# Kernel tuning notes

Measured on AMD Instinct MI355X. Metric: run time of the kernel, lower is better.

## Reference

```python
import jax, jax.numpy as jnp
import numpy as np

N_NODES = 50000
N_EDGES = 400000
IN_DIM = 256
HID = 64
N_CLASSES = 121


def setup_inputs() -> dict:
    key = jax.random.key(0)
    ks = jax.random.split(key, 16)
    inp = {
        "features": jax.random.normal(ks[0], (N_NODES, IN_DIM), jnp.float32),
        "src": jax.random.randint(ks[1], (N_EDGES,), 0, N_NODES, jnp.int32),
        "dst": jax.random.randint(ks[2], (N_EDGES,), 0, N_NODES, jnp.int32),
        # layer 0: 4 heads, in_dim -> hid, no residual
        "W0": jax.random.normal(ks[3], (4, HID, IN_DIM), jnp.float32) * 0.05,
        "al0": jax.random.normal(ks[4], (4, HID), jnp.float32) * 0.05,
        "ar0": jax.random.normal(ks[5], (4, HID), jnp.float32) * 0.05,
        # layer 1: 4 heads, 4*hid -> hid, residual via fc
        "W1": jax.random.normal(ks[6], (4, HID, 4 * HID), jnp.float32) * 0.05,
        "al1": jax.random.normal(ks[7], (4, HID), jnp.float32) * 0.05,
        "ar1": jax.random.normal(ks[8], (4, HID), jnp.float32) * 0.05,
        "R1": jax.random.normal(ks[9], (4, HID, 4 * HID), jnp.float32) * 0.05,
        # final: 6 heads, 4*hid -> classes, residual via fc, averaged
        "Wf": jax.random.normal(ks[10], (6, N_CLASSES, 4 * HID), jnp.float32) * 0.05,
        "alf": jax.random.normal(ks[11], (6, N_CLASSES), jnp.float32) * 0.05,
        "arf": jax.random.normal(ks[12], (6, N_CLASSES), jnp.float32) * 0.05,
        "Rf": jax.random.normal(ks[13], (6, N_CLASSES, 4 * HID), jnp.float32) * 0.05,
    }
    return inp


def _gat_layer(x, src, dst, W, al, ar, R, n_nodes):
    """Multi-head GAT layer. x:[N,D], W:[H,K,D], al/ar:[H,K], R:[H,K,D] or None.
    Returns [N,H,K] = activation(residual + edge-softmax-weighted neighbor sum)."""
    ft = jnp.einsum('nd,hkd->nhk', x, W)              # [N,H,K]
    a1 = jnp.einsum('nhk,hk->nh', ft, al)             # [N,H] attn_l(ft)
    a2 = jnp.einsum('nhk,hk->nh', ft, ar)             # [N,H] attn_r(ft)
    # per-edge score: leaky_relu(a1[dst] + a2[src]) (DGL mailbox softmax over in-edges)
    s = jax.nn.leaky_relu(a1[dst] + a2[src], negative_slope=0.01)   # [E,H]
    smax = jax.ops.segment_max(s, dst, num_segments=n_nodes)        # [N,H]
    smax = jnp.where(jnp.isfinite(smax), smax, 0.0)
    ex = jnp.exp(s - smax[dst])                                     # [E,H]
    denom = jax.ops.segment_sum(ex, dst, num_segments=n_nodes)      # [N,H]
    msg = ex[:, :, None] * ft[src]                                  # [E,H,K]
    accum = jax.ops.segment_sum(msg, dst, num_segments=n_nodes)     # [N,H,K]
    accum = accum / jnp.where(denom > 0, denom, 1.0)[:, :, None]
    if R is not None:
        accum = accum + jnp.einsum('nd,hkd->nhk', x, R)
    return jax.nn.elu(accum)


def reference(features, src, dst, W0, al0, ar0, W1, al1, ar1, R1, Wf, alf, arf, Rf):
    n = features.shape[0]
    h0 = _gat_layer(features, src, dst, W0, al0, ar0, None, n)  # [N,4,64]
    h0 = h0.reshape(n, -1)                                      # concat heads -> [N,256]
    h1 = _gat_layer(h0, src, dst, W1, al1, ar1, R1, n)          # [N,4,64]
    h1 = h1.reshape(n, -1)                                      # [N,256]
    hf = _gat_layer(h1, src, dst, Wf, alf, arf, Rf, n)          # [N,6,121]
    return hf.mean(axis=1)                                      # average final heads -> [N,121]
```

## Files before the change

### kernel.cpp

```cpp
#include <hip/hip_runtime.h>
#include <math.h>

#define NN 50000
#define NE 400000
#define NB ((NN + 255) / 256)

typedef __attribute__((ext_vector_type(8))) short bf16x8;
typedef __attribute__((ext_vector_type(4))) float f32x4;
#define AS1 __attribute__((address_space(1)))
#define AS3 __attribute__((address_space(3)))

__device__ __forceinline__ float lrelu(float x){ return x > 0.0f ? x : 0.01f*x; }
__device__ __forceinline__ float eluf(float x){ return x > 0.0f ? x : __expf(x)-1.0f; }
__device__ __forceinline__ float bf2f(unsigned short u){
  union{unsigned i; float f;} v; v.i = ((unsigned)u)<<16; return v.f;
}
__device__ __forceinline__ unsigned short f2bf(float x){
  union{float f; unsigned i;} v; v.f = x;
  unsigned r = v.i + 0x7FFFu + ((v.i>>16)&1u);
  return (unsigned short)(r>>16);
}
__device__ __forceinline__ unsigned pack2(float a, float b){
  return (unsigned)f2bf(a) | ((unsigned)f2bf(b)<<16);
}
__device__ __forceinline__ float lo16(unsigned u){ return bf2f((unsigned short)(u & 0xffffu)); }
__device__ __forceinline__ float hi16(unsigned u){ return bf2f((unsigned short)(u >> 16)); }

__global__ void k_diag(float* out, float val){ out[0] = val; }

__global__ void k_cvt(const float* __restrict__ in, unsigned short* __restrict__ o, int n){
  int i = (blockIdx.x*256 + threadIdx.x)*4;
  if(i + 3 < n){
    float4 v = *(const float4*)(in + i);
    uint2 p; p.x = pack2(v.x, v.y); p.y = pack2(v.z, v.w);
    *(uint2*)(o + i) = p;
  } else {
    for(int k = i; k < n; k++) o[k] = f2bf(in[k]);
  }
}

__global__ void k_cvt3(const float* __restrict__ s0, const float* __restrict__ s1,
    const float* __restrict__ s2, unsigned short* __restrict__ d0,
    unsigned short* __restrict__ d1, unsigned short* __restrict__ d2, int n){
  const float* in = (blockIdx.y == 0) ? s0 : (blockIdx.y == 1) ? s1 : s2;
  unsigned short* o = (blockIdx.y == 0) ? d0 : (blockIdx.y == 1) ? d1 : d2;
  int i = (blockIdx.x*256 + threadIdx.x)*4;
  if(i + 3 < n){
    float4 v = *(const float4*)(in + i);
    uint2 p; p.x = pack2(v.x, v.y); p.y = pack2(v.z, v.w);
    *(uint2*)(o + i) = p;
  } else {
    for(int k = i; k < n; k++) o[k] = f2bf(in[k]);
  }
}

__global__ void k_cvt2(const float* __restrict__ s0, const float* __restrict__ s1,
    unsigned short* __restrict__ d0, unsigned short* __restrict__ d1, int n){
  const float* in = (blockIdx.y == 0) ? s0 : s1;
  unsigned short* o = (blockIdx.y == 0) ? d0 : d1;
  int i = (blockIdx.x*256 + threadIdx.x)*4;
  if(i + 3 < n){
    float4 v = *(const float4*)(in + i);
    uint2 p; p.x = pack2(v.x, v.y); p.y = pack2(v.z, v.w);
    *(uint2*)(o + i) = p;
  } else {
    for(int k = i; k < n; k++) o[k] = f2bf(in[k]);
  }
}

__global__ void k_foldAll(const float* __restrict__ W0, const float* __restrict__ al0, const float* __restrict__ ar0,
    const float* __restrict__ W1, const float* __restrict__ al1, const float* __restrict__ ar1,
    const float* __restrict__ Wf, const float* __restrict__ alf, const float* __restrict__ arf,
    float* __restrict__ fl0, float* __restrict__ fr0, float* __restrict__ fl1, float* __restrict__ fr1,
    float* __restrict__ flF, float* __restrict__ frF){
  int b = blockIdx.x, d = threadIdx.x;
  const float *W, *al, *ar; float *fl, *fr; int K, h;
  if(b < 4){ W=W0; al=al0; ar=ar0; fl=fl0; fr=fr0; K=64; h=b; }
  else if(b < 8){ W=W1; al=al1; ar=ar1; fl=fl1; fr=fr1; K=64; h=b-4; }
  else { W=Wf; al=alf; ar=arf; fl=flF; fr=frF; K=121; h=b-8; }
  float sl = 0.f, sr = 0.f;
  const float* wb = W + ((size_t)h*K)*256 + d;
  for(int k = 0; k < K; k++){
    float w = wb[(size_t)k*256];
    sl += al[h*K + k]*w;
    sr += ar[h*K + k]*w;
  }
  fl[h*256 + d] = sl;
  fr[h*256 + d] = sr;
}

__global__ void k_count(const int* __restrict__ dst, int* __restrict__ cnt, int E){
  int e = blockIdx.x * 256 + threadIdx.x;
  if(e < E) atomicAdd(&cnt[dst[e]], 1);
}

__global__ void k_scanA(const int* __restrict__ cnt, int* __restrict__ row_ptr,
    int* __restrict__ bsum, int N){
  __shared__ int sh[256];
  int t = threadIdx.x;
  int i = blockIdx.x*256 + t;
  int v = (i < N) ? cnt[i] : 0;
  sh[t] = v;
  __syncthreads();
  for(int off = 1; off < 256; off <<= 1){
    int u = (t >= off) ? sh[t - off] : 0;
    __syncthreads();
    sh[t] += u;
    __syncthreads();
  }
  if(i < N) row_ptr[i] = sh[t] - v;
  if(t == 255) bsum[blockIdx.x] = sh[255];
}

__global__ void k_scanB(const int* __restrict__ bsum, int* __restrict__ boff, int nb){
  __shared__ int sh[256];
  int t = threadIdx.x;
  int v = (t < nb) ? bsum[t] : 0;
  sh[t] = v;
  __syncthreads();
  for(int off = 1; off < 256; off <<= 1){
    int u = (t >= off) ? sh[t - off] : 0;
    __syncthreads();
    sh[t] += u;
    __syncthreads();
  }
  if(t < nb) boff[t] = sh[t] - v;
  if(t == 255) boff[nb] = sh[255];
}

__global__ void k_scanC(int* __restrict__ row_ptr, const int* __restrict__ boff, int N, int nb){
  int i = blockIdx.x*256 + threadIdx.x;
  if(i < N) row_ptr[i] += boff[blockIdx.x];
  if(i == 0) row_ptr[N] = boff[nb];
}

__global__ void k_scatter(const int* __restrict__ src, const int* __restrict__ dst,
    const int* __restrict__ row_ptr, int* __restrict__ cur, int* __restrict__ col_src, int E){
  int e = blockIdx.x * 256 + threadIdx.x;
  if(e < E){
    int d = dst[e];
    int pos = row_ptr[d] + atomicAdd(&cur[d], 1);
    col_src[pos] = src[e];
  }
}

__global__ __launch_bounds__(256) void k_gemm16(const unsigned short* __restrict__ X,
    const unsigned short* __restrict__ W, unsigned short* __restrict__ out,
    int N, int Kout, int ostride){
  __shared__ unsigned short sA[4096];
  __shared__ unsigned short sB[4096];
  int tid = threadIdx.x;
  int l = tid & 63, w = tid >> 6;
  int wm = w >> 1, wn = w & 1;
  int row0 = blockIdx.x*128, col0 = blockIdx.y*128;

  f32x4 acc[4][4];
  #pragma unroll
  for(int i=0;i<4;i++)
    #pragma unroll
    for(int j=0;j<4;j++) acc[i][j] = (f32x4){0.f,0.f,0.f,0.f};

  int grA0 = row0 + l;        if(grA0 >= N) grA0 = 0;
  int grA1 = row0 + 64 + l;   if(grA1 >= N) grA1 = 0;
  int gcB0 = col0 + l;        if(gcB0 >= Kout) gcB0 = 0;
  int gcB1 = col0 + 64 + l;   if(gcB1 >= Kout) gcB1 = 0;
  const unsigned short* pa0 = X + (size_t)grA0*256 + w*8;
  const unsigned short* pa1 = X + (size_t)grA1*256 + w*8;
  const unsigned short* pb0 = W + (size_t)gcB0*256 + w*8;
  const unsigned short* pb1 = W + (size_t)gcB1*256 + w*8;

  AS3 unsigned short* a3A = (AS3 unsigned short*)sA;
  AS3 unsigned short* a3B = (AS3 unsigned short*)sB;

  for(int kt = 0; kt < 256; kt += 32){
    __builtin_amdgcn_global_load_lds((const AS1 void*)(pa0 + kt), (AS3 void*)(a3A + w*1024),       16, 0, 0);
    __builtin_amdgcn_global_load_lds((const AS1 void*)(pa1 + kt), (AS3 void*)(a3A + w*1024 + 512), 16, 0, 0);
    __builtin_amdgcn_global_load_lds((const AS1 void*)(pb0 + kt), (AS3 void*)(a3B + w*1024),       16, 0, 0);
    __builtin_amdgcn_global_load_lds((const AS1 void*)(pb1 + kt), (AS3 void*)(a3B + w*1024 + 512), 16, 0, 0);
    __syncthreads();
    bf16x8 af[4], bfr[4];
    #pragma unroll
    for(int f=0; f<4; f++){
      af[f]  = *(const bf16x8*)(sA + (l>>4)*1024 + (wm*64 + f*16 + (l&15))*8);
      bfr[f] = *(const bf16x8*)(sB + (l>>4)*1024 + (wn*64 + f*16 + (l&15))*8);
    }
    #pragma unroll
    for(int i=0;i<4;i++)
      #pragma unroll
      for(int j=0;j<4;j++)
        acc[i][j] = __builtin_amdgcn_mfma_f32_16x16x32_bf16(af[i], bfr[j], acc[i][j], 0, 0, 0);
    __syncthreads();
  }

  #pragma unroll
  for(int i=0;i<4;i++){
    int rbase = row0 + wm*64 + i*16 + (l>>4)*4;
    #pragma unroll
    for(int j=0;j<4;j++){
      int c = col0 + wn*64 + j*16 + (l&15);
      if(c < Kout){
        #pragma unroll
        for(int q=0;q<4;q++){
          int r = rbase + q;
          if(r < N) out[(size_t)r*ostride + c] = f2bf(acc[i][j][q]);
        }
      }
    }
  }
}

__global__ __launch_bounds__(256) void k_gemmFh(const unsigned short* __restrict__ aggX,
    const unsigned short* __restrict__ xin, const unsigned short* __restrict__ wf,
    const unsigned short* __restrict__ rf, unsigned short* __restrict__ partial, int M){
  __shared__ unsigned short sA[4096];
  __shared__ unsigned short sB[4096];
  int tid = threadIdx.x;
  int l = tid & 63, w = tid >> 6;
  int wm = w >> 1, wn = w & 1;
  int h = blockIdx.y;
  int row0 = blockIdx.x*128;
  int rA0 = row0 + l;      if(rA0 >= M) rA0 = 0;
  int rA1 = row0 + 64 + l; if(rA1 >= M) rA1 = 0;
  int cB1 = 64 + l; if(cB1 > 120) cB1 = 120;

  AS3 unsigned short* a3A = (AS3 unsigned short*)sA;
  AS3 unsigned short* a3B = (AS3 unsigned short*)sB;

  f32x4 acc[4][4];
  #pragma unroll
  for(int i=0;i<4;i++)
    #pragma unroll
    for(int j=0;j<4;j++) acc[i][j] = (f32x4){0.f,0.f,0.f,0.f};

  #pragma unroll 1
  for(int ph = 0; ph < 2; ph++){
    const unsigned short* pa0 = (ph ? xin + (size_t)rA0*256 : aggX + (size_t)rA0*1536 + h*256) + w*8;
    const unsigned short* pa1 = (ph ? xin + (size_t)rA1*256 : aggX + (size_t)rA1*1536 + h*256) + w*8;
    const unsigned short* pbb = (ph ? rf : wf) + (size_t)h*121*256;
    const unsigned short* pb0 = pbb + (size_t)l*256 + w*8;
    const unsigned short* pb1 = pbb + (size_t)cB1*256 + w*8;
    for(int kt = 0; kt < 256; kt += 32){
      __builtin_amdgcn_global_load_lds((const AS1 void*)(pa0 + kt), (AS3 void*)(a3A + w*1024),       16, 0, 0);
      __builtin_amdgcn_global_load_lds((const AS1 void*)(pa1 + kt), (AS3 void*)(a3A + w*1024 + 512), 16, 0, 0);
      __builtin_amdgcn_global_load_lds((const AS1 void*)(pb0 + kt), (AS3 void*)(a3B + w*1024),       16, 0, 0);
      __builtin_amdgcn_global_load_lds((const AS1 void*)(pb1 + kt), (AS3 void*)(a3B + w*1024 + 512), 16, 0, 0);
      __syncthreads();
      bf16x8 af[4], bfr[4];
      #pragma unroll
      for(int f=0; f<4; f++){
        af[f]  = *(const bf16x8*)(sA + (l>>4)*1024 + (wm*64 + f*16 + (l&15))*8);
        bfr[f] = *(const bf16x8*)(sB + (l>>4)*1024 + (wn*64 + f*16 + (l&15))*8);
      }
      #pragma unroll
      for(int i=0;i<4;i++)
        #pragma unroll
        for(int j=0;j<4;j++)
          acc[i][j] = __builtin_amdgcn_mfma_f32_16x16x32_bf16(af[i], bfr[j], acc[i][j], 0, 0, 0);
      __syncthreads();
    }
  }

  unsigned short* pb = partial + (size_t)h*M*128;
  #pragma unroll
  for(int i=0;i<4;i++){
    int rbase = row0 + wm*64 + i*16 + (l>>4)*4;
    #pragma unroll
    for(int j=0;j<4;j++){
      int c = wn*64 + j*16 + (l&15);
      #pragma unroll
      for(int q=0;q<4;q++){
        int r = rbase + q;
        if(r < M) pb[(size_t)r*128 + c] = f2bf(eluf(acc[i][j][q]));
      }
    }
  }
}

__global__ __launch_bounds__(256) void k_reduce6(const unsigned short* __restrict__ partial,
    float* __restrict__ outp, int n0, int M){
  int t = blockIdx.x*256 + threadIdx.x;
  int idx = t >> 7, c = t & 127;
  if(idx >= M || c >= 121) return;
  float s = 0.f;
  #pragma unroll
  for(int h = 0; h < 6; h++) s += bf2f(partial[((size_t)h*M + idx)*128 + c]);
  outp[(size_t)(n0 + idx)*121 + c] = s * (1.0f/6.0f);
}

template<int H, int OS>
__global__ __launch_bounds__(256) void k_a12dot(const unsigned short* __restrict__ x,
    const float* __restrict__ fl, const float* __restrict__ fr,
    float* __restrict__ a1, float* __restrict__ a2){
  int n = blockIdx.x*4 + (threadIdx.x>>6);
  if(n >= NN) return;
  int l = threadIdx.x & 63;
  uint2 rv = *(const uint2*)(x + (size_t)n*256 + l*4);
  float c0 = lo16(rv.x), c1 = hi16(rv.x), c2 = lo16(rv.y), c3 = hi16(rv.y);
  float s1[H], s2[H];
  #pragma unroll
  for(int h = 0; h < H; h++){
    float4 vl = *(const float4*)(fl + h*256 + l*4);
    float4 vr = *(const float4*)(fr + h*256 + l*4);
    s1[h] = c0*vl.x + c1*vl.y + c2*vl.z + c3*vl.w;
    s2[h] = c0*vr.x + c1*vr.y + c2*vr.z + c3*vr.w;
  }
  #pragma unroll
  for(int off = 32; off > 0; off >>= 1){
    #pragma unroll
    for(int h = 0; h < H; h++){
      s1[h] += __shfl_xor(s1[h], off);
      s2[h] += __shfl_xor(s2[h], off);
    }
  }
  if(l == 0){
    #pragma unroll
    for(int h = 0; h < H; h++){ a1[(size_t)n*OS + h] = s1[h]; a2[(size_t)n*OS + h] = s2[h]; }
  }
}

template<bool HAS_RES, int NH, int NOS>
__global__ __launch_bounds__(256) void k_agg4(const unsigned short* __restrict__ ft, int fts,
    const float* __restrict__ a1, const float* __restrict__ a2,
    const int* __restrict__ row_ptr, const int* __restrict__ col_src,
    const unsigned short* __restrict__ res, int rs, unsigned short* __restrict__ outp,
    const float* __restrict__ nfl, const float* __restrict__ nfr,
    float* __restrict__ na1, float* __restrict__ na2){
  int n = blockIdx.x*4 + (threadIdx.x>>6);
  if(n >= NN) return;
  int l = threadIdx.x & 63;
  int h = l >> 4;
  int e0 = row_ptr[n], e1 = row_ptr[n+1];
  float a1v = a1[n*4 + h];
  float acc0=0.f, acc1=0.f, acc2=0.f, acc3=0.f, d=0.f;
  int e = e0;
  for(; e + 4 <= e1; e += 4){
    int s0 = col_src[e], s1 = col_src[e+1], s2 = col_src[e+2], s3 = col_src[e+3];
    float sc0 = a2[(size_t)s0*4 + h];
    float sc1 = a2[(size_t)s1*4 + h];
    float sc2 = a2[(size_t)s2*4 + h];
    float sc3 = a2[(size_t)s3*4 + h];
    uint2 r0 = *(const uint2*)(ft + (size_t)s0*fts + l*4);
    uint2 r1 = *(const uint2*)(ft + (size_t)s1*fts + l*4);
    uint2 r2 = *(const uint2*)(ft + (size_t)s2*fts + l*4);
    uint2 r3 = *(const uint2*)(ft + (size_t)s3*fts + l*4);
    float x0 = __expf(lrelu(a1v + sc0));
    float x1 = __expf(lrelu(a1v + sc1));
    float x2 = __expf(lrelu(a1v + sc2));
    float x3 = __expf(lrelu(a1v + sc3));
    d += (x0 + x1) + (x2 + x3);
    acc0 += x0*lo16(r0.x) + x1*lo16(r1.x) + x2*lo16(r2.x) + x3*lo16(r3.x);
    acc1 += x0*hi16(r0.x) + x1*hi16(r1.x) + x2*hi16(r2.x) + x3*hi16(r3.x);
    acc2 += x0*lo16(r0.y) + x1*lo16(r1.y) + x2*lo16(r2.y) + x3*lo16(r3.y);
    acc3 += x0*hi16(r0.y) + x1*hi16(r1.y) + x2*hi16(r2.y) + x3*hi16(r3.y);
  }
  for(; e < e1; ++e){
    int s = col_src[e];
    float x = __expf(lrelu(a1v + a2[(size_t)s*4 + h]));
    d += x;
    uint2 rv = *(const uint2*)(ft + (size_t)s*fts + l*4);
    acc0 += x*lo16(rv.x); acc1 += x*hi16(rv.x);
    acc2 += x*lo16(rv.y); acc3 += x*hi16(rv.y);
  }
  float inv = (e1 > e0) ? 1.0f/d : 0.0f;
  float v0 = acc0*inv, v1 = acc1*inv, v2 = acc2*inv, v3 = acc3*inv;
  if(HAS_RES){
    uint2 rr = *(const uint2*)(res + (size_t)n*rs + l*4);
    v0 += lo16(rr.x); v1 += hi16(rr.x); v2 += lo16(rr.y); v3 += hi16(rr.y);
  }
  float o0 = eluf(v0), o1 = eluf(v1), o2 = eluf(v2), o3 = eluf(v3);
  uint2 o;
  o.x = pack2(o0, o1);
  o.y = pack2(o2, o3);
  *(uint2*)(outp + (size_t)n*256 + l*4) = o;

  float s1[NH], s2[NH];
  #pragma unroll
  for(int hh = 0; hh < NH; hh++){
    float4 vl = *(const float4*)(nfl + hh*256 + l*4);
    float4 vr = *(const float4*)(nfr + hh*256 + l*4);
    s1[hh] = o0*vl.x + o1*vl.y + o2*vl.z + o3*vl.w;
    s2[hh] = o0*vr.x + o1*vr.y + o2*vr.z + o3*vr.w;
  }
  #pragma unroll
  for(int off = 32; off > 0; off >>= 1){
    #pragma unroll
    for(int hh = 0; hh < NH; hh++){
      s1[hh] += __shfl_xor(s1[hh], off);
      s2[hh] += __shfl_xor(s2[hh], off);
    }
  }
  if(l == 0){
    #pragma unroll
    for(int hh = 0; hh < NH; hh++){
      na1[(size_t)n*NOS + hh] = s1[hh];
      na2[(size_t)n*NOS + hh] = s2[hh];
    }
  }
}

__global__ __launch_bounds__(256) void k_aggx6(const unsigned short* __restrict__ x,
    const float* __restrict__ a1, const float* __restrict__ a2,
    const int* __restrict__ row_ptr, const int* __restrict__ col_src,
    unsigned short* __restrict__ aggX, int n0base, int M){
  int idx = blockIdx.x*4 + (threadIdx.x>>6);
  if(idx >= M) return;
  int n = n0base + idx;
  int l = threadIdx.x & 63;
  int e0 = row_ptr[n], e1 = row_ptr[n+1];
  float a1v[6];
  #pragma unroll
  for(int h=0;h<6;h++) a1v[h] = a1[(size_t)n*8 + h];
  float acc[6][4];
  float d[6];
  #pragma unroll
  for(int h=0;h<6;h++){ d[h]=0.f; acc[h][0]=0.f; acc[h][1]=0.f; acc[h][2]=0.f; acc[h][3]=0.f; }
  int e = e0;
  for(; e + 2 <= e1; e += 2){
    int s0 = col_src[e], s1 = col_src[e+1];
    float4 alo0 = *(const float4*)(a2 + (size_t)s0*8);
    float2 ahi0 = *(const float2*)(a2 + (size_t)s0*8 + 4);
    float4 alo1 = *(const float4*)(a2 + (size_t)s1*8);
    float2 ahi1 = *(const float2*)(a2 + (size_t)s1*8 + 4);
    uint2 rv0 = *(const uint2*)(x + (size_t)s0*256 + l*4);
    uint2 rv1 = *(const uint2*)(x + (size_t)s1*256 + l*4);
    float ex0[6], ex1[6];
    ex0[0] = __expf(lrelu(a1v[0] + alo0.x));
    ex0[1] = __expf(lrelu(a1v[1] + alo0.y));
    ex0[2] = __expf(lrelu(a1v[2] + alo0.z));
    ex0[3] = __expf(lrelu(a1v[3] + alo0.w));
    ex0[4] = __expf(lrelu(a1v[4] + ahi0.x));
    ex0[5] = __expf(lrelu(a1v[5] + ahi0.y));
    ex1[0] = __expf(lrelu(a1v[0] + alo1.x));
    ex1[1] = __expf(lrelu(a1v[1] + alo1.y));
    ex1[2] = __expf(lrelu(a1v[2] + alo1.z));
    ex1[3] = __expf(lrelu(a1v[3] + alo1.w));
    ex1[4] = __expf(lrelu(a1v[4] + ahi1.x));
    ex1[5] = __expf(lrelu(a1v[5] + ahi1.y));
    float c00 = lo16(rv0.x), c01 = hi16(rv0.x), c02 = lo16(rv0.y), c03 = hi16(rv0.y);
    float c10 = lo16(rv1.x), c11 = hi16(rv1.x), c12 = lo16(rv1.y), c13 = hi16(rv1.y);
    #pragma unroll
    for(int h=0;h<6;h++){
      d[h] += ex0[h] + ex1[h];
      acc[h][0] += ex0[h]*c00 + ex1[h]*c10;
      acc[h][1] += ex0[h]*c01 + ex1[h]*c11;
      acc[h][2] += ex0[h]*c02 + ex1[h]*c12;
      acc[h][3] += ex0[h]*c03 + ex1[h]*c13;
    }
  }
  for(; e < e1; ++e){
    int s = col_src[e];
    float4 alo = *(const float4*)(a2 + (size_t)s*8);
    float2 ahi = *(const float2*)(a2 + (size_t)s*8 + 4);
    uint2 rv = *(const uint2*)(x + (size_t)s*256 + l*4);
    float ex[6];
    ex[0] = __expf(lrelu(a1v[0] + alo.x));
    ex[1] = __expf(lrelu(a1v[1] + alo.y));
    ex[2] = __expf(lrelu(a1v[2] + alo.z));
    ex[3] = __expf(lrelu(a1v[3] + alo.w));
    ex[4] = __expf(lrelu(a1v[4] + ahi.x));
    ex[5] = __expf(lrelu(a1v[5] + ahi.y));
    float c0 = lo16(rv.x), c1 = hi16(rv.x), c2 = lo16(rv.y), c3 = hi16(rv.y);
    #pragma unroll
    for(int h=0;h<6;h++){
      d[h] += ex[h];
      acc[h][0] += ex[h]*c0;
      acc[h][1] += ex[h]*c1;
      acc[h][2] += ex[h]*c2;
      acc[h][3] += ex[h]*c3;
    }
  }
  bool deg = e1 > e0;
  #pragma unroll
  for(int h=0;h<6;h++){
    float inv = deg ? 1.0f/d[h] : 0.0f;
    uint2 o;
    o.x = pack2(acc[h][0]*inv, acc[h][1]*inv);
    o.y = pack2(acc[h][2]*inv, acc[h][3]*inv);
    *(uint2*)(aggX + (size_t)idx*1536 + h*256 + l*4) = o;
  }
}

extern "C" void kernel_launch(void* const* d_in, const int* in_sizes, int n_in,
                              void* d_out, int out_size, void* d_ws, size_t ws_size,
                              hipStream_t stream){
  const float* features = (const float*)d_in[0];
  const int*   src      = (const int*)d_in[1];
  const int*   dst      = (const int*)d_in[2];
  const float* W0  = (const float*)d_in[3];
  const float* al0 = (const float*)d_in[4];
  const float* ar0 = (const float*)d_in[5];
  const float* W1  = (const float*)d_in[6];
  const float* al1 = (const float*)d_in[7];
  const float* ar1 = (const float*)d_in[8];
  const float* R1  = (const float*)d_in[9];
  const float* Wf  = (const float*)d_in[10];
  const float* alf = (const float*)d_in[11];
  const float* arf = (const float*)d_in[12];
  const float* Rf  = (const float*)d_in[13];
  float* out = (float*)d_out;
  (void)in_sizes; (void)n_in; (void)out_size;

  char* ws = (char*)d_ws;
  size_t off = 0;
  auto take = [&](size_t bytes) -> void* {
    void* p = ws + off;
    off += (bytes + 255) & ~(size_t)255;
    return p;
  };
  const int CH = 25000;
  int* row_ptr = (int*)take((NN + 1) * sizeof(int));
  int* cur     = (int*)take(NN * sizeof(int));
  int* col_src = (int*)take(NE * sizeof(int));
  int* bsum    = (int*)take(256 * sizeof(int));
  int* boff    = (int*)take(257 * sizeof(int));
  float* a1A = (float*)take((size_t)NN * 8 * sizeof(float));
  float* a2A = (float*)take((size_t)NN * 8 * sizeof(float));
  float* a1B = (float*)take((size_t)NN * 8 * sizeof(float));
  float* a2B = (float*)take((size_t)NN * 8 * sizeof(float));
  unsigned short* ftres  = (unsigned short*)take((size_t)NN * 512 * 2);
  unsigned short* feat16 = (unsigned short*)take((size_t)NN * 256 * 2);
  unsigned short* hA16   = (unsigned short*)take((size_t)NN * 256 * 2);
  unsigned short* hB16   = (unsigned short*)take((size_t)NN * 256 * 2);
  unsigned short* aggX   = (unsigned short*)take((size_t)CH * 1536 * 2);
  unsigned short* w016  = (unsigned short*)take(65536 * 2);
  unsigned short* w1r1  = (unsigned short*)take(131072 * 2);
  unsigned short* wf16  = (unsigned short*)take(185856 * 2);
  unsigned short* rf16  = (unsigned short*)take(185856 * 2);
  float* fl0 = (float*)take(4*256*sizeof(float));
  float* fr0 = (float*)take(4*256*sizeof(float));
  float* fl1 = (float*)take(4*256*sizeof(float));
  float* fr1 = (float*)take(4*256*sizeof(float));
  float* flF = (float*)take(6*256*sizeof(float));
  float* frF = (float*)take(6*256*sizeof(float));
  size_t need = off;

  if(ws_size < need){
    k_diag<<<1, 1, 0, stream>>>(out, 100.0f + (float)((double)ws_size / 1073741824.0));
    return;
  }

  unsigned short* partialF = ftres;

  hipMemsetAsync(cur, 0, NN * sizeof(int), stream);
  k_count<<<(NE + 255)/256, 256, 0, stream>>>(dst, cur, NE);
  k_scanA<<<NB, 256, 0, stream>>>(cur, row_ptr, bsum, NN);
  k_scanB<<<1, 256, 0, stream>>>(bsum, boff, NB);
  k_scanC<<<NB, 256, 0, stream>>>(row_ptr, boff, NN, NB);
  hipMemsetAsync(cur, 0, NN * sizeof(int), stream);
  k_scatter<<<(NE + 255)/256, 256, 0, stream>>>(src, dst, row_ptr, cur, col_src, NE);

  k_cvt<<<(NN*256/4 + 255)/256, 256, 0, stream>>>(features, feat16, NN*256);
  k_cvt3<<<dim3(64, 3), 256, 0, stream>>>(W0, W1, R1, w016, w1r1, w1r1 + 65536, 65536);
  k_cvt2<<<dim3(182, 2), 256, 0, stream>>>(Wf, Rf, wf16, rf16, 185856);
  k_foldAll<<<14, 256, 0, stream>>>(W0, al0, ar0, W1, al1, ar1, Wf, alf, arf,
                                    fl0, fr0, fl1, fr1, flF, frF);

  int gm = (NN + 127) / 128;
  int gagg = (NN + 3) / 4;

  k_a12dot<4,4><<<gagg, 256, 0, stream>>>(feat16, fl0, fr0, a1A, a2A);
  k_gemm16<<<dim3(gm, 2), 256, 0, stream>>>(feat16, w016, ftres, NN, 256, 256);
  k_agg4<false,4,4><<<gagg, 256, 0, stream>>>(ftres, 256, a1A, a2A, row_ptr, col_src,
      nullptr, 0, hA16, fl1, fr1, a1B, a2B);

  k_gemm16<<<dim3(gm, 4), 256, 0, stream>>>(hA16, w1r1, ftres, NN, 512, 512);
  k_agg4<true,6,8><<<gagg, 256, 0, stream>>>(ftres, 512, a1B, a2B, row_ptr, col_src,
      ftres + 256, 512, hB16, flF, frF, a1A, a2A);

  for(int c = 0; c < 2; c++){
    int n0 = c*CH;
    k_aggx6<<<(CH + 3)/4, 256, 0, stream>>>(hB16, a1A, a2A, row_ptr, col_src, aggX, n0, CH);
    k_gemmFh<<<dim3((CH + 127)/128, 6), 256, 0, stream>>>(aggX, hB16 + (size_t)n0*256, wf16, rf16, partialF, CH);
    k_reduce6<<<(CH*128 + 255)/256, 256, 0, stream>>>(partialF, out, n0, CH);
  }
}
```

Measured before the change: 517.7 us.

## Precompute per-edge attention exps and fuse final head averaging via atomics

Adds a per-edge kernel that computes exp(leaky_relu(a1[dst]+a2[src])) once into a contiguous CSR-ordered buffer, using a new col_dst array. The aggregation kernels then read these values sequentially instead of gathering a2 per source and recomputing exp in every lane. The final layer drops the two-chunk loop and the k_reduce6 pass. k_gemmFh now atomically adds ELU(acc)/6 into a zeroed output and uses a 64-wide K tile. The trade-offs are three extra edge passes, more workspace, and non-deterministic float atomic accumulation order.

```diff
diff --git a/kernel.cpp b/kernel.cpp
--- a/kernel.cpp
+++ b/kernel.cpp
@@ -135,12 +135,47 @@
 }
 
 __global__ void k_scatter(const int* __restrict__ src, const int* __restrict__ dst,
-    const int* __restrict__ row_ptr, int* __restrict__ cur, int* __restrict__ col_src, int E){
+    const int* __restrict__ row_ptr, int* __restrict__ cur,
+    int* __restrict__ col_src, int* __restrict__ col_dst, int E){
   int e = blockIdx.x * 256 + threadIdx.x;
   if(e < E){
     int d = dst[e];
     int pos = row_ptr[d] + atomicAdd(&cur[d], 1);
     col_src[pos] = src[e];
+    col_dst[pos] = d;
+  }
+}
+
+template<int S>
+__global__ __launch_bounds__(256) void k_eexp(const int* __restrict__ col_src, const int* __restrict__ col_dst,
+    const float* __restrict__ a1, const float* __restrict__ a2, float* __restrict__ ex){
+  int p = blockIdx.x*256 + threadIdx.x;
+  if(p >= NE) return;
+  int s = col_src[p], d = col_dst[p];
+  if(S == 4){
+    float4 v1 = *(const float4*)(a1 + (size_t)d*4);
+    float4 v2 = *(const float4*)(a2 + (size_t)s*4);
+    float4 o;
+    o.x = __expf(lrelu(v1.x + v2.x));
+    o.y = __expf(lrelu(v1.y + v2.y));
+    o.z = __expf(lrelu(v1.z + v2.z));
+    o.w = __expf(lrelu(v1.w + v2.w));
+    *(float4*)(ex + (size_t)p*4) = o;
+  } else {
+    float4 l1 = *(const float4*)(a1 + (size_t)d*8);
+    float2 h1 = *(const float2*)(a1 + (size_t)d*8 + 4);
+    float4 l2 = *(const float4*)(a2 + (size_t)s*8);
+    float2 h2 = *(const float2*)(a2 + (size_t)s*8 + 4);
+    float4 o;
+    o.x = __expf(lrelu(l1.x + l2.x));
+    o.y = __expf(lrelu(l1.y + l2.y));
+    o.z = __expf(lrelu(l1.z + l2.z));
+    o.w = __expf(lrelu(l1.w + l2.w));
+    float2 o2;
+    o2.x = __expf(lrelu(h1.x + h2.x));
+    o2.y = __expf(lrelu(h1.y + h2.y));
+    *(float4*)(ex + (size_t)p*8) = o;
+    *(float2*)(ex + (size_t)p*8 + 4) = o2;
   }
 }
 
@@ -211,9 +246,9 @@
 
 __global__ __launch_bounds__(256) void k_gemmFh(const unsigned short* __restrict__ aggX,
     const unsigned short* __restrict__ xin, const unsigned short* __restrict__ wf,
-    const unsigned short* __restrict__ rf, unsigned short* __restrict__ partial, int M){
-  __shared__ unsigned short sA[4096];
-  __shared__ unsigned short sB[4096];
+    const unsigned short* __restrict__ rf, float* __restrict__ outp, int M){
+  __shared__ unsigned short sA[8192];
+  __shared__ unsigned short sB[8192];
   int tid = threadIdx.x;
   int l = tid & 63, w = tid >> 6;
   int wm = w >> 1, wn = w & 1;
@@ -239,52 +274,52 @@
     const unsigned short* pbb = (ph ? rf : wf) + (size_t)h*121*256;
     const unsigned short* pb0 = pbb + (size_t)l*256 + w*8;
     const unsigned short* pb1 = pbb + (size_t)cB1*256 + w*8;
-    for(int kt = 0; kt < 256; kt += 32){
-      __builtin_amdgcn_global_load_lds((const AS1 void*)(pa0 + kt), (AS3 void*)(a3A + w*1024),       16, 0, 0);
-      __builtin_amdgcn_global_load_lds((const AS1 void*)(pa1 + kt), (AS3 void*)(a3A + w*1024 + 512), 16, 0, 0);
-      __builtin_amdgcn_global_load_lds((const AS1 void*)(pb0 + kt), (AS3 void*)(a3B + w*1024),       16, 0, 0);
-      __builtin_amdgcn_global_load_lds((const AS1 void*)(pb1 + kt), (AS3 void*)(a3B + w*1024 + 512), 16, 0, 0);
+    #pragma unroll 1
+    for(int kt = 0; kt < 256; kt += 64){
+      #pragma unroll
+      for(int jj = 0; jj < 2; jj++){
+        int j = w + jj*4;
+        int ko = kt + jj*32;
+        __builtin_amdgcn_global_load_lds((const AS1 void*)(pa0 + ko), (AS3 void*)(a3A + j*1024),       16, 0, 0);
+        __builtin_amdgcn_global_load_lds((const AS1 void*)(pa1 + ko), (AS3 void*)(a3A + j*1024 + 512), 16, 0, 0);
+        __builtin_amdgcn_global_load_lds((const AS1 void*)(pb0 + ko), (AS3 void*)(a3B + j*1024),       16, 0, 0);
+        __builtin_amdgcn_global_load_lds((const AS1 void*)(pb1 + ko), (AS3 void*)(a3B + j*1024 + 512), 16, 0, 0);
+      }
       __syncthreads();
-      bf16x8 af[4], bfr[4];
       #pragma unroll
-      for(int f=0; f<4; f++){
-        af[f]  = *(const bf16x8*)(sA + (l>>4)*1024 + (wm*64 + f*16 + (l&15))*8);
-        bfr[f] = *(const bf16x8*)(sB + (l>>4)*1024 + (wn*64 + f*16 + (l&15))*8);
+      for(int ks = 0; ks < 2; ks++){
+        bf16x8 af[4], bfr[4];
+        #pragma unroll
+        for(int f=0; f<4; f++){
+          af[f]  = *(const bf16x8*)(sA + (ks*4 + (l>>4))*1024 + (wm*64 + f*16 + (l&15))*8);
+          bfr[f] = *(const bf16x8*)(sB + (ks*4 + (l>>4))*1024 + (wn*64 + f*16 + (l&15))*8);
+        }
+        #pragma unroll
+        for(int i=0;i<4;i++)
+          #pragma unroll
+          for(int j=0;j<4;j++)
+            acc[i][j] = __builtin_amdgcn_mfma_f32_16x16x32_bf16(af[i], bfr[j], acc[i][j], 0, 0, 0);
       }
-      #pragma unroll
-      for(int i=0;i<4;i++)
-        #pragma unroll
-        for(int j=0;j<4;j++)
-          acc[i][j] = __builtin_amdgcn_mfma_f32_16x16x32_bf16(af[i], bfr[j], acc[i][j], 0, 0, 0);
       __syncthreads();
     }
   }
 
-  unsigned short* pb = partial + (size_t)h*M*128;
+  const float inv6 = 1.0f/6.0f;
   #pragma unroll
   for(int i=0;i<4;i++){
     int rbase = row0 + wm*64 + i*16 + (l>>4)*4;
     #pragma unroll
     for(int j=0;j<4;j++){
       int c = wn*64 + j*16 + (l&15);
-      #pragma unroll
-      for(int q=0;q<4;q++){
-        int r = rbase + q;
-        if(r < M) pb[(size_t)r*128 + c] = f2bf(eluf(acc[i][j][q]));
+      if(c < 121){
+        #pragma unroll
+        for(int q=0;q<4;q++){
+          int r = rbase + q;
+          if(r < M) atomicAdd(&outp[(size_t)r*121 + c], eluf(acc[i][j][q]) * inv6);
+        }
       }
     }
   }
-}
-
-__global__ __launch_bounds__(256) void k_reduce6(const unsigned short* __restrict__ partial,
-    float* __restrict__ outp, int n0, int M){
-  int t = blockIdx.x*256 + threadIdx.x;
-  int idx = t >> 7, c = t & 127;
-  if(idx >= M || c >= 121) return;
-  float s = 0.f;
-  #pragma unroll
-  for(int h = 0; h < 6; h++) s += bf2f(partial[((size_t)h*M + idx)*128 + c]);
-  outp[(size_t)(n0 + idx)*121 + c] = s * (1.0f/6.0f);
 }
 
 template<int H, int OS>
@@ -320,7 +355,7 @@
 
 template<bool HAS_RES, int NH, int NOS>
 __global__ __launch_bounds__(256) void k_agg4(const unsigned short* __restrict__ ft, int fts,
-    const float* __restrict__ a1, const float* __restrict__ a2,
+    const float* __restrict__ ex4,
     const int* __restrict__ row_ptr, const int* __restrict__ col_src,
     const unsigned short* __restrict__ res, int rs, unsigned short* __restrict__ outp,
     const float* __restrict__ nfl, const float* __restrict__ nfr,
@@ -330,23 +365,18 @@
   int l = threadIdx.x & 63;
   int h = l >> 4;
   int e0 = row_ptr[n], e1 = row_ptr[n+1];
-  float a1v = a1[n*4 + h];
   float acc0=0.f, acc1=0.f, acc2=0.f, acc3=0.f, d=0.f;
   int e = e0;
   for(; e + 4 <= e1; e += 4){
     int s0 = col_src[e], s1 = col_src[e+1], s2 = col_src[e+2], s3 = col_src[e+3];
-    float sc0 = a2[(size_t)s0*4 + h];
-    float sc1 = a2[(size_t)s1*4 + h];
-    float sc2 = a2[(size_t)s2*4 + h];
-    float sc3 = a2[(size_t)s3*4 + h];
+    float x0 = ex4[(size_t)(e+0)*4 + h];
+    float x1 = ex4[(size_t)(e+1)*4 + h];
+    float x2 = ex4[(size_t)(e+2)*4 + h];
+    float x3 = ex4[(size_t)(e+3)*4 + h];
     uint2 r0 = *(const uint2*)(ft + (size_t)s0*fts + l*4);
     uint2 r1 = *(const uint2*)(ft + (size_t)s1*fts + l*4);
     uint2 r2 = *(const uint2*)(ft + (size_t)s2*fts + l*4);
     uint2 r3 = *(const uint2*)(ft + (size_t)s3*fts + l*4);
-    float x0 = __expf(lrelu(a1v + sc0));
-    float x1 = __expf(lrelu(a1v + sc1));
-    float x2 = __expf(lrelu(a1v + sc2));
-    float x3 = __expf(lrelu(a1v + sc3));
     d += (x0 + x1) + (x2 + x3);
     acc0 += x0*lo16(r0.x) + x1*lo16(r1.x) + x2*lo16(r2.x) + x3*lo16(r3.x);
     acc1 += x0*hi16(r0.x) + x1*hi16(r1.x) + x2*hi16(r2.x) + x3*hi16(r3.x);
@@ -355,7 +385,7 @@
   }
   for(; e < e1; ++e){
     int s = col_src[e];
-    float x = __expf(lrelu(a1v + a2[(size_t)s*4 + h]));
+    float x = ex4[(size_t)e*4 + h];
     d += x;
     uint2 rv = *(const uint2*)(ft + (size_t)s*fts + l*4);
     acc0 += x*lo16(rv.x); acc1 += x*hi16(rv.x);
@@ -399,17 +429,13 @@
 }
 
 __global__ __launch_bounds__(256) void k_aggx6(const unsigned short* __restrict__ x,
-    const float* __restrict__ a1, const float* __restrict__ a2,
+    const float* __restrict__ ex6,
     const int* __restrict__ row_ptr, const int* __restrict__ col_src,
-    unsigned short* __restrict__ aggX, int n0base, int M){
-  int idx = blockIdx.x*4 + (threadIdx.x>>6);
-  if(idx >= M) return;
-  int n = n0base + idx;
+    unsigned short* __restrict__ aggX){
+  int n = blockIdx.x*4 + (threadIdx.x>>6);
+  if(n >= NN) return;
   int l = threadIdx.x & 63;
   int e0 = row_ptr[n], e1 = row_ptr[n+1];
-  float a1v[6];
-  #pragma unroll
-  for(int h=0;h<6;h++) a1v[h] = a1[(size_t)n*8 + h];
   float acc[6][4];
   float d[6];
   #pragma unroll
@@ -417,25 +443,14 @@
   int e = e0;
   for(; e + 2 <= e1; e += 2){
     int s0 = col_src[e], s1 = col_src[e+1];
-    float4 alo0 = *(const float4*)(a2 + (size_t)s0*8);
-    float2 ahi0 = *(const float2*)(a2 + (size_t)s0*8 + 4);
-    float4 alo1 = *(const float4*)(a2 + (size_t)s1*8);
-    float2 ahi1 = *(const float2*)(a2 + (size_t)s1*8 + 4);
+    float4 xl0 = *(const float4*)(ex6 + (size_t)(e+0)*8);
+    float2 xh0 = *(const float2*)(ex6 + (size_t)(e+0)*8 + 4);
+    float4 xl1 = *(const float4*)(ex6 + (size_t)(e+1)*8);
+    float2 xh1 = *(const float2*)(ex6 + (size_t)(e+1)*8 + 4);
     uint2 rv0 = *(const uint2*)(x + (size_t)s0*256 + l*4);
     uint2 rv1 = *(const uint2*)(x + (size_t)s1*256 + l*4);
-    float ex0[6], ex1[6];
-    ex0[0] = __expf(lrelu(a1v[0] + alo0.x));
-    ex0[1] = __expf(lrelu(a1v[1] + alo0.y));
-    ex0[2] = __expf(lrelu(a1v[2] + alo0.z));
-    ex0[3] = __expf(lrelu(a1v[3] + alo0.w));
-    ex0[4] = __expf(lrelu(a1v[4] + ahi0.x));
-    ex0[5] = __expf(lrelu(a1v[5] + ahi0.y));
-    ex1[0] = __expf(lrelu(a1v[0] + alo1.x));
-    ex1[1] = __expf(lrelu(a1v[1] + alo1.y));
-    ex1[2] = __expf(lrelu(a1v[2] + alo1.z));
-    ex1[3] = __expf(lrelu(a1v[3] + alo1.w));
-    ex1[4] = __expf(lrelu(a1v[4] + ahi1.x));
-    ex1[5] = __expf(lrelu(a1v[5] + ahi1.y));
+    float ex0[6] = {xl0.x, xl0.y, xl0.z, xl0.w, xh0.x, xh0.y};
+    float ex1[6] = {xl1.x, xl1.y, xl1.z, xl1.w, xh1.x, xh1.y};
     float c00 = lo16(rv0.x), c01 = hi16(rv0.x), c02 = lo16(rv0.y), c03 = hi16(rv0.y);
     float c10 = lo16(rv1.x), c11 = hi16(rv1.x), c12 = lo16(rv1.y), c13 = hi16(rv1.y);
     #pragma unroll
@@ -449,24 +464,18 @@
   }
   for(; e < e1; ++e){
     int s = col_src[e];
-    float4 alo = *(const float4*)(a2 + (size_t)s*8);
-    float2 ahi = *(const float2*)(a2 + (size_t)s*8 + 4);
+    float4 xl = *(const float4*)(ex6 + (size_t)e*8);
+    float2 xh = *(const float2*)(ex6 + (size_t)e*8 + 4);
     uint2 rv = *(const uint2*)(x + (size_t)s*256 + l*4);
-    float ex[6];
-    ex[0] = __expf(lrelu(a1v[0] + alo.x));
-    ex[1] = __expf(lrelu(a1v[1] + alo.y));
-    ex[2] = __expf(lrelu(a1v[2] + alo.z));
-    ex[3] = __expf(lrelu(a1v[3] + alo.w));
-    ex[4] = __expf(lrelu(a1v[4] + ahi.x));
-    ex[5] = __expf(lrelu(a1v[5] + ahi.y));
+    float exv[6] = {xl.x, xl.y, xl.z, xl.w, xh.x, xh.y};
     float c0 = lo16(rv.x), c1 = hi16(rv.x), c2 = lo16(rv.y), c3 = hi16(rv.y);
     #pragma unroll
     for(int h=0;h<6;h++){
-      d[h] += ex[h];
-      acc[h][0] += ex[h]*c0;
-      acc[h][1] += ex[h]*c1;
-      acc[h][2] += ex[h]*c2;
-      acc[h][3] += ex[h]*c3;
+      d[h] += exv[h];
+      acc[h][0] += exv[h]*c0;
+      acc[h][1] += exv[h]*c1;
+      acc[h][2] += exv[h]*c2;
+      acc[h][3] += exv[h]*c3;
     }
   }
   bool deg = e1 > e0;
@@ -476,7 +485,7 @@
     uint2 o;
     o.x = pack2(acc[h][0]*inv, acc[h][1]*inv);
     o.y = pack2(acc[h][2]*inv, acc[h][3]*inv);
-    *(uint2*)(aggX + (size_t)idx*1536 + h*256 + l*4) = o;
+    *(uint2*)(aggX + (size_t)n*1536 + h*256 + l*4) = o;
   }
 }
 
@@ -507,21 +516,23 @@
     off += (bytes + 255) & ~(size_t)255;
     return p;
   };
-  const int CH = 25000;
   int* row_ptr = (int*)take((NN + 1) * sizeof(int));
   int* cur     = (int*)take(NN * sizeof(int));
   int* col_src = (int*)take(NE * sizeof(int));
+  int* col_dst = (int*)take(NE * sizeof(int));
   int* bsum    = (int*)take(256 * sizeof(int));
   int* boff    = (int*)take(257 * sizeof(int));
   float* a1A = (float*)take((size_t)NN * 8 * sizeof(float));
   float* a2A = (float*)take((size_t)NN * 8 * sizeof(float));
   float* a1B = (float*)take((size_t)NN * 8 * sizeof(float));
   float* a2B = (float*)take((size_t)NN * 8 * sizeof(float));
+  unsigned short* hB16   = (unsigned short*)take((size_t)NN * 256 * 2);
   unsigned short* ftres  = (unsigned short*)take((size_t)NN * 512 * 2);
   unsigned short* feat16 = (unsigned short*)take((size_t)NN * 256 * 2);
   unsigned short* hA16   = (unsigned short*)take((size_t)NN * 256 * 2);
-  unsigned short* hB16   = (unsigned short*)take((size_t)NN * 256 * 2);
-  unsigned short* aggX   = (unsigned short*)take((size_t)CH * 1536 * 2);
+  unsigned short* aggtl  = (unsigned short*)take((size_t)NN * 512 * 2);
+  float* ex4 = (float*)take((size_t)NE * 4 * sizeof(float));
+  float* ex6 = (float*)take((size_t)NE * 8 * sizeof(float));
   unsigned short* w016  = (unsigned short*)take(65536 * 2);
   unsigned short* w1r1  = (unsigned short*)take(131072 * 2);
   unsigned short* wf16  = (unsigned short*)take(185856 * 2);
@@ -533,13 +544,14 @@
   float* flF = (float*)take(6*256*sizeof(float));
   float* frF = (float*)take(6*256*sizeof(float));
   size_t need = off;
+  (void)aggtl;
 
   if(ws_size < need){
     k_diag<<<1, 1, 0, stream>>>(out, 100.0f + (float)((double)ws_size / 1073741824.0));
     return;
   }
 
-  unsigned short* partialF = ftres;
+  unsigned short* aggX = ftres;
 
   hipMemsetAsync(cur, 0, NN * sizeof(int), stream);
   k_count<<<(NE + 255)/256, 256, 0, stream>>>(dst, cur, NE);
@@ -547,7 +559,7 @@
   k_scanB<<<1, 256, 0, stream>>>(bsum, boff, NB);
   k_scanC<<<NB, 256, 0, stream>>>(row_ptr, boff, NN, NB);
   hipMemsetAsync(cur, 0, NN * sizeof(int), stream);
-  k_scatter<<<(NE + 255)/256, 256, 0, stream>>>(src, dst, row_ptr, cur, col_src, NE);
+  k_scatter<<<(NE + 255)/256, 256, 0, stream>>>(src, dst, row_ptr, cur, col_src, col_dst, NE);
 
   k_cvt<<<(NN*256/4 + 255)/256, 256, 0, stream>>>(features, feat16, NN*256);
   k_cvt3<<<dim3(64, 3), 256, 0, stream>>>(W0, W1, R1, w016, w1r1, w1r1 + 65536, 65536);
@@ -557,20 +569,21 @@
 
   int gm = (NN + 127) / 128;
   int gagg = (NN + 3) / 4;
+  int gedge = (NE + 255) / 256;
 
   k_a12dot<4,4><<<gagg, 256, 0, stream>>>(feat16, fl0, fr0, a1A, a2A);
+  k_eexp<4><<<gedge, 256, 0, stream>>>(col_src, col_dst, a1A, a2A, ex4);
   k_gemm16<<<dim3(gm, 2), 256, 0, stream>>>(feat16, w016, ftres, NN, 256, 256);
-  k_agg4<false,4,4><<<gagg, 256, 0, stream>>>(ftres, 256, a1A, a2A, row_ptr, col_src,
+  k_agg4<false,4,4><<<gagg, 256, 0, stream>>>(ftres, 256, ex4, row_ptr, col_src,
       nullptr, 0, hA16, fl1, fr1, a1B, a2B);
 
+  k_eexp<4><<<gedge, 256, 0, stream>>>(col_src, col_dst, a1B, a2B, ex4);
   k_gemm16<<<dim3(gm, 4), 256, 0, stream>>>(hA16, w1r1, ftres, NN, 512, 512);
-  k_agg4<true,6,8><<<gagg, 256, 0, stream>>>(ftres, 512, a1B, a2B, row_ptr, col_src,
+  k_agg4<true,6,8><<<gagg, 256, 0, stream>>>(ftres, 512, ex4, row_ptr, col_src,
       ftres + 256, 512, hB16, flF, frF, a1A, a2A);
 
-  for(int c = 0; c < 2; c++){
-    int n0 = c*CH;
-    k_aggx6<<<(CH + 3)/4, 256, 0, stream>>>(hB16, a1A, a2A, row_ptr, col_src, aggX, n0, CH);
-    k_gemmFh<<<dim3((CH + 127)/128, 6), 256, 0, stream>>>(aggX, hB16 + (size_t)n0*256, wf16, rf16, partialF, CH);
-    k_reduce6<<<(CH*128 + 255)/256, 256, 0, stream>>>(partialF, out, n0, CH);
-  }
-}
+  k_eexp<8><<<gedge, 256, 0, stream>>>(col_src, col_dst, a1A, a2A, ex6);
+  k_aggx6<<<gagg, 256, 0, stream>>>(hB16, ex6, row_ptr, col_src, aggX);
+  hipMemsetAsync(out, 0, (size_t)NN * 121 * sizeof(float), stream);
+  k_gemmFh<<<dim3(gm, 6), 256, 0, stream>>>(aggX, hB16, wf16, rf16, out, NN);
+}
```

Result: slower. 636.4 us (+22.9%).
